# Kernel tuning notes

Hardware: AMD Instinct MI355X
Metric: run time of the kernel (lower is better)

The kernel has to match this reference:

```python
import jax, jax.numpy as jnp
import numpy as np

N_NODES = 50000
N_EDGES = 800000
IN_C, HID, OUT_C, N_LAYERS = 32, 64, 8, 3

def _init(key, fan_in, shape):
    return jax.random.normal(key, shape, dtype=jnp.float32) * (1.0 / np.sqrt(fan_in))

def setup_inputs() -> dict:
    key = jax.random.key(0)
    ks = jax.random.split(key, 16)
    x = jax.random.uniform(ks[0], (N_NODES, IN_C), dtype=jnp.float32)
    edge_index = jax.random.randint(ks[1], (2, N_EDGES), 0, N_NODES, dtype=jnp.int64)
    return {
        "x": x,
        "edge_index": edge_index,
        # encoder MLP: in -> hid -> hid
        "enc_w1": _init(ks[2], IN_C, (IN_C, HID)),
        "enc_b1": jnp.zeros((HID,), jnp.float32),
        "enc_w2": _init(ks[3], HID, (HID, HID)),
        "enc_b2": jnp.zeros((HID,), jnp.float32),
        # stacked SAGEConv params: lin_l (aggregated neighbors, has bias) and lin_r (root)
        "sage_wl": _init(ks[4], HID, (N_LAYERS, HID, HID)),
        "sage_wr": _init(ks[5], HID, (N_LAYERS, HID, HID)),
        "sage_b": jnp.zeros((N_LAYERS, HID), jnp.float32),
        # decoder MLP: hid -> hid -> out
        "dec_w1": _init(ks[6], HID, (HID, HID)),
        "dec_b1": jnp.zeros((HID,), jnp.float32),
        "dec_w2": _init(ks[7], HID, (HID, OUT_C)),
        "dec_b2": jnp.zeros((OUT_C,), jnp.float32),
    }

def _gelu(x):
    return jax.nn.gelu(x, approximate=False)  # torch.nn.GELU default = exact erf

def reference(x, edge_index, enc_w1, enc_b1, enc_w2, enc_b2,
              sage_wl, sage_wr, sage_b, dec_w1, dec_b1, dec_w2, dec_b2):
    n = x.shape[0]
    src, dst = edge_index[0], edge_index[1]  # messages flow src -> dst (PyG convention)
    # in-degree counts for mean aggregation (computed once)
    deg = jax.ops.segment_sum(jnp.ones((src.shape[0],), x.dtype), dst, num_segments=n)
    inv_deg = 1.0 / jnp.maximum(deg, 1.0)

    # encoder MLP (Linear -> GELU -> Linear)
    h = _gelu(x @ enc_w1 + enc_b1) @ enc_w2 + enc_b2

    # SAGEConv + GELU blocks
    for l in range(sage_wl.shape[0]):
        agg = jax.ops.segment_sum(h[src], dst, num_segments=n) * inv_deg[:, None]
        h = _gelu(agg @ sage_wl[l] + h @ sage_wr[l] + sage_b[l])

    # decoder MLP
    out = _gelu(h @ dec_w1 + dec_b1) @ dec_w2 + dec_b2
    return out
```

## Files before the change

### kernel.cpp

```cpp
#include <hip/hip_runtime.h>
#include <math.h>

#define NN 50000
#define NE 800000
#define INC 32
#define HIDC 64
#define OUTC 8
#define NT_TILES ((NN + 63) / 64)
#define NPAD (NT_TILES * 64)
#define AS 68
#define XS 36
#define NCH 250
#define ECHK (NE / NCH)
#define NBK2 196

__device__ __forceinline__ float gelu_exact(float x){
    return 0.5f * x * (1.0f + erff(x * 0.70710678118654752f));
}

template<int ST, int KK>
__device__ __forceinline__ void mm_tile(const float* __restrict__ At,
                                        const float* __restrict__ Ws,
                                        int m0, int n0, float acc[4][4])
{
    #pragma unroll 2
    for (int k = 0; k < KK; k += 2){
        float2 av[4];
        #pragma unroll
        for (int r = 0; r < 4; r++)
            av[r] = *(const float2*)&At[(m0+r)*ST + k];
        float4 w0 = *(const float4*)&Ws[(k+0)*HIDC + n0];
        float4 w1 = *(const float4*)&Ws[(k+1)*HIDC + n0];
        #pragma unroll
        for (int r = 0; r < 4; r++){
            acc[r][0] = fmaf(av[r].x, w0.x, acc[r][0]);
            acc[r][1] = fmaf(av[r].x, w0.y, acc[r][1]);
            acc[r][2] = fmaf(av[r].x, w0.z, acc[r][2]);
            acc[r][3] = fmaf(av[r].x, w0.w, acc[r][3]);
            acc[r][0] = fmaf(av[r].y, w1.x, acc[r][0]);
            acc[r][1] = fmaf(av[r].y, w1.y, acc[r][1]);
            acc[r][2] = fmaf(av[r].y, w1.z, acc[r][2]);
            acc[r][3] = fmaf(av[r].y, w1.w, acc[r][3]);
        }
    }
}


__global__ __launch_bounds__(256) void k_ebin(
    const int* __restrict__ src, const int* __restrict__ dst,
    int2* __restrict__ ebuf, int* __restrict__ cnts, int* __restrict__ lboff)
{
    __shared__ int cnt[256];
    __shared__ int cur[256];
    int c = blockIdx.x, tid = threadIdx.x;
    cnt[tid] = 0;
    __syncthreads();
    int e0 = c*ECHK;
    for (int i = e0 + tid; i < e0 + ECHK; i += 256)
        atomicAdd(&cnt[dst[i] >> 8], 1);
    __syncthreads();
    int v = cnt[tid];
    for (int off = 1; off < 256; off <<= 1){
        int t = (tid >= off) ? cnt[tid-off] : 0;
        __syncthreads();
        cnt[tid] += t;
        __syncthreads();
    }
    int excl = cnt[tid] - v;
    if (tid < NBK2){
        cnts[c*NBK2 + tid]  = v;
        lboff[c*NBK2 + tid] = excl;
    }
    cur[tid] = excl;
    __syncthreads();
    for (int i = e0 + tid; i < e0 + ECHK; i += 256){
        int d = dst[i], s = src[i];
        int p = atomicAdd(&cur[d >> 8], 1);
        ebuf[e0 + p] = make_int2(d, s);
    }
}

__global__ __launch_bounds__(256) void k_choff(
    const int* __restrict__ cnts, int* __restrict__ choff, int* __restrict__ btot)
{
    __shared__ int sd[256];
    int b = blockIdx.x, tid = threadIdx.x;
    int v = (tid < NCH) ? cnts[tid*NBK2 + b] : 0;
    sd[tid] = v;
    __syncthreads();
    for (int off = 1; off < 256; off <<= 1){
        int t = (tid >= off) ? sd[tid-off] : 0;
        __syncthreads();
        sd[tid] += t;
        __syncthreads();
    }
    if (tid < NCH) choff[b*NCH + tid] = sd[tid] - v;
    if (tid == 255) btot[b] = sd[255];
}

__global__ __launch_bounds__(256) void k_bbase(
    const int* __restrict__ btot, int* __restrict__ bbase,
    float* h0, float* h1, int* row_ptr)
{
    __shared__ int sd[256];
    int tid = threadIdx.x;
    int v = (tid < NBK2) ? btot[tid] : 0;
    sd[tid] = v;
    __syncthreads();
    for (int off = 1; off < 256; off <<= 1){
        int t = (tid >= off) ? sd[tid-off] : 0;
        __syncthreads();
        sd[tid] += t;
        __syncthreads();
    }
    if (tid < NBK2) bbase[tid] = sd[tid] - v;
    if (tid == 0) row_ptr[NN] = NE;
    if (tid < 64){
        h0[(size_t)NN*HIDC + tid] = 0.f;
        h1[(size_t)NN*HIDC + tid] = 0.f;
    }
}

__global__ __launch_bounds__(256) void k_bsort(
    const int2* __restrict__ ebuf, const int* __restrict__ lboff,
    const int* __restrict__ choff, const int* __restrict__ btot,
    const int* __restrict__ bbase,
    int* __restrict__ row_ptr, int* __restrict__ col,
    float* __restrict__ inv_deg)
{
    __shared__ int cum[NCH];
    __shared__ int lb[NCH];
    __shared__ int hcnt[256];
    __shared__ int fpos[256];
    int b = blockIdx.x, tid = threadIdx.x;
    if (tid < NCH){
        cum[tid] = choff[b*NCH + tid];
        lb[tid]  = lboff[tid*NBK2 + b];
    }
    hcnt[tid] = 0;
    __syncthreads();
    int tot = btot[b];
    int lo = b << 8;
    for (int e = tid; e < tot; e += 256){
        int lc = 0, hc = NCH;
        while (hc - lc > 1){ int mid = (lc+hc) >> 1; if (cum[mid] <= e) lc = mid; else hc = mid; }
        int2 pr = ebuf[lc*ECHK + lb[lc] + (e - cum[lc])];
        atomicAdd(&hcnt[pr.x - lo], 1);
    }
    __syncthreads();
    int v = hcnt[tid];
    for (int off = 1; off < 256; off <<= 1){
        int t = (tid >= off) ? hcnt[tid-off] : 0;
        __syncthreads();
        hcnt[tid] += t;
        __syncthreads();
    }
    int excl = hcnt[tid] - v;
    int base = bbase[b];
    int g = lo + tid;
    if (g < NN){
        row_ptr[g] = base + excl;
        inv_deg[g] = 1.0f / (float)max(v, 1);
    }
    fpos[tid] = base + excl;
    __syncthreads();
    for (int e = tid; e < tot; e += 256){
        int lc = 0, hc = NCH;
        while (hc - lc > 1){ int mid = (lc+hc) >> 1; if (cum[mid] <= e) lc = mid; else hc = mid; }
        int2 pr = ebuf[lc*ECHK + lb[lc] + (e - cum[lc])];
        int q = atomicAdd(&fpos[pr.x - lo], 1);
        col[q] = pr.y;
    }
}

__global__ __launch_bounds__(256) void k_agg(
    const float* __restrict__ h_in,
    const int* __restrict__ row_ptr, const int* __restrict__ col,
    const float* __restrict__ inv_deg,
    float* __restrict__ agg)
{
    int tid = threadIdx.x;
    int wv = tid >> 6, f = tid & 63;
    int g = f >> 4, qoff = (f & 15) * 4;
    for (int node = blockIdx.x*4 + wv; node < NN; node += gridDim.x*4){
        int s0 = row_ptr[node], s1 = row_ptr[node+1];
        float a0 = 0.f, a1 = 0.f, a2 = 0.f, a3 = 0.f;
        for (int p0 = s0; p0 < s1; p0 += 64){
            int cnt = s1 - p0; if (cnt > 64) cnt = 64;
            int cidx = (f < cnt) ? col[p0 + f] : NN;
            int nq = (cnt + 3) >> 2;
            for (int t = 0; t < nq; t++){
                int sidx = __shfl(cidx, t*4 + g);
                float4 v = *(const float4*)&h_in[(size_t)sidx*HIDC + qoff];
                a0 += v.x; a1 += v.y; a2 += v.z; a3 += v.w;
            }
        }
        a0 += __shfl_xor(a0, 16); a0 += __shfl_xor(a0, 32);
        a1 += __shfl_xor(a1, 16); a1 += __shfl_xor(a1, 32);
        a2 += __shfl_xor(a2, 16); a2 += __shfl_xor(a2, 32);
        a3 += __shfl_xor(a3, 16); a3 += __shfl_xor(a3, 32);
        if (g == 0){
            float idg = inv_deg[node];
            float4 o = make_float4(a0*idg, a1*idg, a2*idg, a3*idg);
            *(float4*)&agg[(size_t)node*HIDC + qoff] = o;
        }
    }
}


__global__ __launch_bounds__(256) void k_enc(
    const float* __restrict__ x,
    const float* __restrict__ w1, const float* __restrict__ b1,
    const float* __restrict__ w2, const float* __restrict__ b2,
    float* __restrict__ h)
{
    __shared__ float w1s[INC*HIDC];
    __shared__ float w2s[HIDC*HIDC];
    __shared__ float Xt[64*XS];
    __shared__ float T[64*AS];
    int tid = threadIdx.x, tile = blockIdx.x;
    for (int i = tid*4; i < INC*HIDC;  i += 1024)
        *(float4*)&w1s[i] = *(const float4*)&w1[i];
    for (int i = tid*4; i < HIDC*HIDC; i += 1024)
        *(float4*)&w2s[i] = *(const float4*)&w2[i];
    for (int i = tid*4; i < 64*INC; i += 1024){
        int m = i >> 5, k = i & 31;
        int row = tile*64 + m; if (row >= NN) row = NN-1;
        *(float4*)&Xt[m*XS + k] = *(const float4*)&x[(size_t)row*INC + k];
    }
    __syncthreads();
    int tx = tid & 15, ty = tid >> 4;
    int m0 = ty*4, n0 = tx*4;
    float4 b1v = *(const float4*)&b1[n0];
    float acc[4][4];
    #pragma unroll
    for (int r = 0; r < 4; r++){
        acc[r][0]=b1v.x; acc[r][1]=b1v.y; acc[r][2]=b1v.z; acc[r][3]=b1v.w;
    }
    mm_tile<XS, INC>(Xt, w1s, m0, n0, acc);
    #pragma unroll
    for (int r = 0; r < 4; r++){
        float4 o = make_float4(gelu_exact(acc[r][0]), gelu_exact(acc[r][1]),
                               gelu_exact(acc[r][2]), gelu_exact(acc[r][3]));
        *(float4*)&T[(m0+r)*AS + n0] = o;
    }
    __syncthreads();
    float4 b2v = *(const float4*)&b2[n0];
    #pragma unroll
    for (int r = 0; r < 4; r++){
        acc[r][0]=b2v.x; acc[r][1]=b2v.y; acc[r][2]=b2v.z; acc[r][3]=b2v.w;
    }
    mm_tile<AS, HIDC>(T, w2s, m0, n0, acc);
    #pragma unroll
    for (int r = 0; r < 4; r++){
        int node = tile*64 + m0 + r;
        if (node < NN)
            *(float4*)&h[(size_t)node*HIDC + n0] =
                make_float4(acc[r][0], acc[r][1], acc[r][2], acc[r][3]);
    }
}

__global__ __launch_bounds__(256) void k_sage(
    const float* __restrict__ h_in, const float* __restrict__ agg,
    const float* __restrict__ wl, const float* __restrict__ wr,
    const float* __restrict__ bias, float* __restrict__ h_out)
{
    __shared__ float Wl[HIDC*HIDC];
    __shared__ float Wr[HIDC*HIDC];
    __shared__ float At[64*AS];
    int tid = threadIdx.x, tile = blockIdx.x;
    for (int i = tid*4; i < HIDC*HIDC; i += 1024){
        *(float4*)&Wl[i] = *(const float4*)&wl[i];
        *(float4*)&Wr[i] = *(const float4*)&wr[i];
    }
    const float* abase = agg + (size_t)tile*64*HIDC;
    for (int i = tid*4; i < 64*HIDC; i += 1024){
        int m = i >> 6, k = i & 63;
        *(float4*)&At[m*AS + k] = *(const float4*)&abase[i];
    }
    __syncthreads();
    int tx = tid & 15, ty = tid >> 4;
    int m0 = ty*4, n0 = tx*4;
    float4 bv = *(const float4*)&bias[n0];
    float acc[4][4];
    #pragma unroll
    for (int r = 0; r < 4; r++){
        acc[r][0]=bv.x; acc[r][1]=bv.y; acc[r][2]=bv.z; acc[r][3]=bv.w;
    }
    mm_tile<AS, HIDC>(At, Wl, m0, n0, acc);
    __syncthreads();
    const float* hbase = h_in + (size_t)tile*64*HIDC;
    for (int i = tid*4; i < 64*HIDC; i += 1024){
        int m = i >> 6, k = i & 63;
        *(float4*)&At[m*AS + k] = *(const float4*)&hbase[i];
    }
    __syncthreads();
    mm_tile<AS, HIDC>(At, Wr, m0, n0, acc);
    #pragma unroll
    for (int r = 0; r < 4; r++){
        int node = tile*64 + m0 + r;
        if (node < NN)
            *(float4*)&h_out[(size_t)node*HIDC + n0] =
                make_float4(gelu_exact(acc[r][0]), gelu_exact(acc[r][1]),
                            gelu_exact(acc[r][2]), gelu_exact(acc[r][3]));
    }
}

__global__ __launch_bounds__(256) void k_dec(
    const float* __restrict__ hbuf,
    const float* __restrict__ w1, const float* __restrict__ b1,
    const float* __restrict__ w2, const float* __restrict__ b2,
    float* __restrict__ out)
{
    __shared__ float w1s[HIDC*HIDC];
    __shared__ float w2s[HIDC*OUTC];
    __shared__ float At[64*AS];
    __shared__ float T[64*AS];
    int tid = threadIdx.x, tile = blockIdx.x;
    for (int i = tid*4; i < HIDC*HIDC; i += 1024)
        *(float4*)&w1s[i] = *(const float4*)&w1[i];
    if (tid*4 < HIDC*OUTC)
        *(float4*)&w2s[tid*4] = *(const float4*)&w2[tid*4];
    const float* hbase = hbuf + (size_t)tile*64*HIDC;
    for (int i = tid*4; i < 64*HIDC; i += 1024){
        int m = i >> 6, k = i & 63;
        *(float4*)&At[m*AS + k] = *(const float4*)&hbase[i];
    }
    __syncthreads();
    int tx = tid & 15, ty = tid >> 4;
    int m0 = ty*4, n0 = tx*4;
    float4 b1v = *(const float4*)&b1[n0];
    float acc[4][4];
    #pragma unroll
    for (int r = 0; r < 4; r++){
        acc[r][0]=b1v.x; acc[r][1]=b1v.y; acc[r][2]=b1v.z; acc[r][3]=b1v.w;
    }
    mm_tile<AS, HIDC>(At, w1s, m0, n0, acc);
    #pragma unroll
    for (int r = 0; r < 4; r++){
        float4 o = make_float4(gelu_exact(acc[r][0]), gelu_exact(acc[r][1]),
                               gelu_exact(acc[r][2]), gelu_exact(acc[r][3]));
        *(float4*)&T[(m0+r)*AS + n0] = o;
    }
    __syncthreads();
    int m = tid >> 2, c0 = (tid & 3) * 2;
    float a0 = b2[c0], a1 = b2[c0+1];
    #pragma unroll 4
    for (int k = 0; k < HIDC; k++){
        float tv = T[m*AS + k];
        float2 wv = *(const float2*)&w2s[k*OUTC + c0];
        a0 = fmaf(tv, wv.x, a0);
        a1 = fmaf(tv, wv.y, a1);
    }
    int node = tile*64 + m;
    if (node < NN)
        *(float2*)&out[(size_t)node*OUTC + c0] = make_float2(a0, a1);
}

extern "C" void kernel_launch(void* const* d_in, const int* in_sizes, int n_in,
                              void* d_out, int out_size, void* d_ws, size_t ws_size,
                              hipStream_t stream){
    const float* x      = (const float*)d_in[0];
    const int*   ei     = (const int*)  d_in[1];
    const float* enc_w1 = (const float*)d_in[2];
    const float* enc_b1 = (const float*)d_in[3];
    const float* enc_w2 = (const float*)d_in[4];
    const float* enc_b2 = (const float*)d_in[5];
    const float* sage_wl= (const float*)d_in[6];
    const float* sage_wr= (const float*)d_in[7];
    const float* sage_b = (const float*)d_in[8];
    const float* dec_w1 = (const float*)d_in[9];
    const float* dec_b1 = (const float*)d_in[10];
    const float* dec_w2 = (const float*)d_in[11];
    const float* dec_b2 = (const float*)d_in[12];
    float* out = (float*)d_out;

    char* ws = (char*)d_ws;
    size_t off = 0;
    auto alloc = [&](size_t bytes)->void*{
        void* p = ws + off; off = (off + bytes + 255) & ~(size_t)255; return p;
    };
    int*   cnts     = (int*)  alloc((size_t)NCH*NBK2*4);
    int*   lboff    = (int*)  alloc((size_t)NCH*NBK2*4);
    int*   choff    = (int*)  alloc((size_t)NBK2*NCH*4);
    int*   btot     = (int*)  alloc((size_t)NBK2*4);
    int*   bbase    = (int*)  alloc((size_t)NBK2*4);
    int*   row_ptr  = (int*)  alloc((size_t)(NN+1)*4);
    int*   col      = (int*)  alloc((size_t)NE*4);
    float* inv_deg  = (float*)alloc((size_t)NN*4);
    float* h0       = (float*)alloc((size_t)NPAD*HIDC*4);
    float* h1       = (float*)alloc((size_t)NPAD*HIDC*4);
    float* agg      = (float*)alloc((size_t)NPAD*HIDC*4);
    int2*  ebuf     = (int2*)agg;

    const int* srcv = ei;
    const int* dstv = ei + NE;

    hipLaunchKernelGGL(k_ebin,  dim3(NCH),  dim3(256), 0, stream,
                       srcv, dstv, ebuf, cnts, lboff);
    hipLaunchKernelGGL(k_choff, dim3(NBK2), dim3(256), 0, stream,
                       cnts, choff, btot);
    hipLaunchKernelGGL(k_bbase, dim3(1),    dim3(256), 0, stream,
                       btot, bbase, h0, h1, row_ptr);
    hipLaunchKernelGGL(k_bsort, dim3(NBK2), dim3(256), 0, stream,
                       ebuf, lboff, choff, btot, bbase, row_ptr, col, inv_deg);

    hipLaunchKernelGGL(k_enc, dim3(NT_TILES), dim3(256), 0, stream,
                       x, enc_w1, enc_b1, enc_w2, enc_b2, h0);

    const float* hin = h0; float* hout = h1;
    for (int l = 0; l < 3; l++){
        hipLaunchKernelGGL(k_agg, dim3(2048), dim3(256), 0, stream,
                           hin, row_ptr, col, inv_deg, agg);
        hipLaunchKernelGGL(k_sage, dim3(NT_TILES), dim3(256), 0, stream,
                           hin, agg,
                           sage_wl + (size_t)l*HIDC*HIDC,
                           sage_wr + (size_t)l*HIDC*HIDC,
                           sage_b  + (size_t)l*HIDC,
                           hout);
        float* t = (float*)hin; hin = hout; hout = t;
    }

    hipLaunchKernelGGL(k_dec, dim3(NT_TILES), dim3(256), 0, stream,
                       hin, dec_w1, dec_b1, dec_w2, dec_b2, out);
}
```

Before: 243.9 us.

## Use 128-node buckets and cache edges in registers during bucket sort

Halves the destination-bucket width to 128 nodes, doubling the bucket count to 391, and widens the binning and base-scan kernels to 512 threads to match. In the bucket-sort kernel each thread keeps up to 12 edges in registers from the counting pass, so the scatter pass no longer repeats the binary search and the ebuf read for them. This is meant to double the parallelism of the bucket sort and cut its redundant global loads, at the cost of more registers and more per-chunk count traffic in the offset kernels.

```diff
diff --git a/kernel.cpp b/kernel.cpp
--- a/kernel.cpp
+++ b/kernel.cpp
@@ -12,7 +12,9 @@
 #define XS 36
 #define NCH 250
 #define ECHK (NE / NCH)
-#define NBK2 196
+#define BKD 128
+#define NBK2 ((NN + BKD - 1) / BKD)
+#define EC 12
 
 __device__ __forceinline__ float gelu_exact(float x){
     return 0.5f * x * (1.0f + erff(x * 0.70710678118654752f));
@@ -46,21 +48,21 @@
 }
 
 
-__global__ __launch_bounds__(256) void k_ebin(
+__global__ __launch_bounds__(512) void k_ebin(
     const int* __restrict__ src, const int* __restrict__ dst,
     int2* __restrict__ ebuf, int* __restrict__ cnts, int* __restrict__ lboff)
 {
-    __shared__ int cnt[256];
-    __shared__ int cur[256];
+    __shared__ int cnt[512];
+    __shared__ int cur[512];
     int c = blockIdx.x, tid = threadIdx.x;
     cnt[tid] = 0;
     __syncthreads();
     int e0 = c*ECHK;
-    for (int i = e0 + tid; i < e0 + ECHK; i += 256)
-        atomicAdd(&cnt[dst[i] >> 8], 1);
+    for (int i = e0 + tid; i < e0 + ECHK; i += 512)
+        atomicAdd(&cnt[dst[i] >> 7], 1);
     __syncthreads();
     int v = cnt[tid];
-    for (int off = 1; off < 256; off <<= 1){
+    for (int off = 1; off < 512; off <<= 1){
         int t = (tid >= off) ? cnt[tid-off] : 0;
         __syncthreads();
         cnt[tid] += t;
@@ -73,9 +75,9 @@
     }
     cur[tid] = excl;
     __syncthreads();
-    for (int i = e0 + tid; i < e0 + ECHK; i += 256){
+    for (int i = e0 + tid; i < e0 + ECHK; i += 512){
         int d = dst[i], s = src[i];
-        int p = atomicAdd(&cur[d >> 8], 1);
+        int p = atomicAdd(&cur[d >> 7], 1);
         ebuf[e0 + p] = make_int2(d, s);
     }
 }
@@ -98,16 +100,16 @@
     if (tid == 255) btot[b] = sd[255];
 }
 
-__global__ __launch_bounds__(256) void k_bbase(
+__global__ __launch_bounds__(512) void k_bbase(
     const int* __restrict__ btot, int* __restrict__ bbase,
     float* h0, float* h1, int* row_ptr)
 {
-    __shared__ int sd[256];
+    __shared__ int sd[512];
     int tid = threadIdx.x;
     int v = (tid < NBK2) ? btot[tid] : 0;
     sd[tid] = v;
     __syncthreads();
-    for (int off = 1; off < 256; off <<= 1){
+    for (int off = 1; off < 512; off <<= 1){
         int t = (tid >= off) ? sd[tid-off] : 0;
         __syncthreads();
         sd[tid] += t;
@@ -130,41 +132,63 @@
 {
     __shared__ int cum[NCH];
     __shared__ int lb[NCH];
-    __shared__ int hcnt[256];
-    __shared__ int fpos[256];
+    __shared__ int hcnt[BKD];
+    __shared__ int fpos[BKD];
     int b = blockIdx.x, tid = threadIdx.x;
     if (tid < NCH){
         cum[tid] = choff[b*NCH + tid];
         lb[tid]  = lboff[tid*NBK2 + b];
     }
-    hcnt[tid] = 0;
+    if (tid < BKD) hcnt[tid] = 0;
     __syncthreads();
     int tot = btot[b];
-    int lo = b << 8;
-    for (int e = tid; e < tot; e += 256){
+    int lo = b << 7;
+    int dl[EC], sv[EC];
+    #pragma unroll
+    for (int j = 0; j < EC; j++){
+        int e = tid + j*256;
+        dl[j] = -1; sv[j] = 0;
+        if (e < tot){
+            int lc = 0, hc = NCH;
+            while (hc - lc > 1){ int mid = (lc+hc) >> 1; if (cum[mid] <= e) lc = mid; else hc = mid; }
+            int2 pr = ebuf[lc*ECHK + lb[lc] + (e - cum[lc])];
+            dl[j] = pr.x - lo; sv[j] = pr.y;
+            atomicAdd(&hcnt[dl[j]], 1);
+        }
+    }
+    for (int e = tid + EC*256; e < tot; e += 256){
         int lc = 0, hc = NCH;
         while (hc - lc > 1){ int mid = (lc+hc) >> 1; if (cum[mid] <= e) lc = mid; else hc = mid; }
         int2 pr = ebuf[lc*ECHK + lb[lc] + (e - cum[lc])];
         atomicAdd(&hcnt[pr.x - lo], 1);
     }
     __syncthreads();
-    int v = hcnt[tid];
-    for (int off = 1; off < 256; off <<= 1){
-        int t = (tid >= off) ? hcnt[tid-off] : 0;
-        __syncthreads();
-        hcnt[tid] += t;
-        __syncthreads();
-    }
-    int excl = hcnt[tid] - v;
+    int v = (tid < BKD) ? hcnt[tid] : 0;
+    for (int off = 1; off < BKD; off <<= 1){
+        int t = (tid >= off && tid < BKD) ? hcnt[tid-off] : 0;
+        __syncthreads();
+        if (tid < BKD) hcnt[tid] += t;
+        __syncthreads();
+    }
     int base = bbase[b];
-    int g = lo + tid;
-    if (g < NN){
-        row_ptr[g] = base + excl;
-        inv_deg[g] = 1.0f / (float)max(v, 1);
-    }
-    fpos[tid] = base + excl;
-    __syncthreads();
-    for (int e = tid; e < tot; e += 256){
+    if (tid < BKD){
+        int excl = hcnt[tid] - v;
+        int g = lo + tid;
+        if (g < NN){
+            row_ptr[g] = base + excl;
+            inv_deg[g] = 1.0f / (float)max(v, 1);
+        }
+        fpos[tid] = base + excl;
+    }
+    __syncthreads();
+    #pragma unroll
+    for (int j = 0; j < EC; j++){
+        if (dl[j] >= 0){
+            int q = atomicAdd(&fpos[dl[j]], 1);
+            col[q] = sv[j];
+        }
+    }
+    for (int e = tid + EC*256; e < tot; e += 256){
         int lc = 0, hc = NCH;
         while (hc - lc > 1){ int mid = (lc+hc) >> 1; if (cum[mid] <= e) lc = mid; else hc = mid; }
         int2 pr = ebuf[lc*ECHK + lb[lc] + (e - cum[lc])];
@@ -396,11 +420,11 @@
     const int* srcv = ei;
     const int* dstv = ei + NE;
 
-    hipLaunchKernelGGL(k_ebin,  dim3(NCH),  dim3(256), 0, stream,
+    hipLaunchKernelGGL(k_ebin,  dim3(NCH),  dim3(512), 0, stream,
                        srcv, dstv, ebuf, cnts, lboff);
     hipLaunchKernelGGL(k_choff, dim3(NBK2), dim3(256), 0, stream,
                        cnts, choff, btot);
-    hipLaunchKernelGGL(k_bbase, dim3(1),    dim3(256), 0, stream,
+    hipLaunchKernelGGL(k_bbase, dim3(1),    dim3(512), 0, stream,
                        btot, bbase, h0, h1, row_ptr);
     hipLaunchKernelGGL(k_bsort, dim3(NBK2), dim3(256), 0, stream,
                        ebuf, lboff, choff, btot, bbase, row_ptr, col, inv_deg);
```

New measurement: 225.8 us. 7.4% less time.
